# Kernel tuning notes

Hardware: AMD Instinct MI355X
Metric: run time of the kernel (lower is better)

## Reference

```python
import jax, jax.numpy as jnp
import numpy as np

N_QUBITS = 4
N_LAYERS = 2
BATCH = 262144


def _apply_ry(psi, theta, wire):
    # psi: (B, 2,2,2,2) real statevector; theta: scalar or (B,)
    c = jnp.reshape(jnp.cos(theta * 0.5), (-1, 1, 1, 1))
    s = jnp.reshape(jnp.sin(theta * 0.5), (-1, 1, 1, 1))
    psi = jnp.moveaxis(psi, wire + 1, 1)
    a, b = psi[:, 0], psi[:, 1]
    psi = jnp.stack([c * a - s * b, s * a + c * b], axis=1)
    return jnp.moveaxis(psi, 1, wire + 1)


def _apply_cnot(psi, ctrl, tgt):
    # flip target amplitude where control bit is 1
    psi = jnp.moveaxis(psi, (ctrl + 1, tgt + 1), (1, 2))
    psi = psi.at[:, 1].set(psi[:, 1, ::-1])
    return jnp.moveaxis(psi, (1, 2), (ctrl + 1, tgt + 1))


def _circuit(encoded, q_params):
    # Batched 4-qubit statevector sim (RY/CNOT are real matrices -> real psi).
    B = encoded.shape[0]
    psi = jnp.zeros((B, 2 ** N_QUBITS), encoded.dtype).at[:, 0].set(1.0)
    psi = psi.reshape((B,) + (2,) * N_QUBITS)  # wire 0 = most significant axis
    for w in range(N_QUBITS):
        psi = _apply_ry(psi, encoded[:, w], w)
    for layer in range(N_LAYERS):
        for i in range(N_QUBITS - 1):
            psi = _apply_cnot(psi, i, i + 1)
        psi = _apply_cnot(psi, N_QUBITS - 1, 0)  # ring closure (n_qubits > 2)
        for i in range(N_QUBITS):
            psi = _apply_ry(psi, q_params[layer * N_QUBITS + i], i)
    p = psi * psi  # probabilities
    zs = []
    for w in range(N_QUBITS):
        pw = jnp.moveaxis(p, w + 1, 1).reshape(B, 2, -1)
        zs.append(pw[:, 0].sum(-1) - pw[:, 1].sum(-1))  # <Z_w>
    return jnp.stack(zs, axis=-1)  # (B, 4)


def setup_inputs() -> dict:
    key = jax.random.key(0)
    ks = jax.random.split(key, 10)
    f32 = jnp.float32
    state = jax.random.normal(ks[0], (BATCH, 64), dtype=f32)
    # state_encoder: Linear(64,32) -> ReLU -> Linear(32,4) -> Tanh
    W1 = jax.random.normal(ks[1], (32, 64), dtype=f32) / np.sqrt(64.0)
    b1 = jnp.zeros((32,), f32)
    W2 = jax.random.normal(ks[2], (N_QUBITS, 32), dtype=f32) / np.sqrt(32.0)
    b2 = jnp.zeros((N_QUBITS,), f32)
    q_params = jax.random.normal(ks[3], (N_LAYERS * N_QUBITS,), dtype=f32) * 0.1
    # q_value_head: Linear(4,32) -> ReLU -> Linear(32,16) -> Tanh
    H1 = jax.random.normal(ks[4], (32, N_QUBITS), dtype=f32) / np.sqrt(float(N_QUBITS))
    c1 = jnp.zeros((32,), f32)
    H2 = jax.random.normal(ks[5], (16, 32), dtype=f32) / np.sqrt(32.0)
    c2 = jnp.zeros((16,), f32)
    return {"state": state, "W1": W1, "b1": b1, "W2": W2, "b2": b2,
            "q_params": q_params, "H1": H1, "c1": c1, "H2": H2, "c2": c2}


def reference(state, W1, b1, W2, b2, q_params, H1, c1, H2, c2):
    B = state.shape[0]
    x = state.reshape(B, -1)
    h = jax.nn.relu(x @ W1.T + b1)
    encoded = jnp.tanh(h @ W2.T + b2)            # (B, 4) rotation angles
    qf = _circuit(encoded, q_params)             # (B, 4) PauliZ expectations
    h2 = jax.nn.relu(qf @ H1.T + c1)
    q_values = jnp.tanh(h2 @ H2.T + c2)          # (B, 16)
    return q_values.reshape(B, 4, 4)
```

## Files before the change

kernel.cpp:

```cpp
#include <hip/hip_runtime.h>

#define TPB 256
#define BATCH 262144
#define S 34
#define EST 10
#define H2ST 36

typedef __fp16   fp16x2  __attribute__((ext_vector_type(2)));
typedef _Float16 half8_t __attribute__((ext_vector_type(8)));
typedef float    f32x4   __attribute__((ext_vector_type(4)));

#define WAVE_LDS_FENCE() asm volatile("s_waitcnt lgkmcnt(0)" ::: "memory")

__device__ __forceinline__ float fast_tanh(float x) {
    float ax = fabsf(x);
    float e  = __expf(-2.0f * ax);
    float t  = (1.0f - e) * __builtin_amdgcn_rcpf(1.0f + e);
    return copysignf(t, x);
}

template <int MASK>
__device__ __forceinline__ void ry_gate(float* psi, float c, float s) {
#pragma unroll
    for (int i = 0; i < 16; i++) {
        if (!(i & MASK)) {
            float a = psi[i], b = psi[i | MASK];
            psi[i]        = c * a - s * b;
            psi[i | MASK] = s * a + c * b;
        }
    }
}

template <int CM, int TM>
__device__ __forceinline__ void cnot_gate(float* psi) {
#pragma unroll
    for (int i = 0; i < 16; i++) {
        if ((i & CM) && !(i & TM)) {
            float t = psi[i];
            psi[i] = psi[i | TM];
            psi[i | TM] = t;
        }
    }
}

__device__ __forceinline__ half8_t cvt8(float4 a, float4 b) {
    fp16x2 p0 = __builtin_amdgcn_cvt_pkrtz(a.x, a.y);
    fp16x2 p1 = __builtin_amdgcn_cvt_pkrtz(a.z, a.w);
    fp16x2 p2 = __builtin_amdgcn_cvt_pkrtz(b.x, b.y);
    fp16x2 p3 = __builtin_amdgcn_cvt_pkrtz(b.z, b.w);
    half8_t r;
    r[0] = (_Float16)p0[0]; r[1] = (_Float16)p0[1];
    r[2] = (_Float16)p1[0]; r[3] = (_Float16)p1[1];
    r[4] = (_Float16)p2[0]; r[5] = (_Float16)p2[1];
    r[6] = (_Float16)p3[0]; r[7] = (_Float16)p3[1];
    return r;
}

__device__ __forceinline__ half8_t cvt8_rne(float4 a, float4 b) {
    half8_t r;
    r[0] = (_Float16)a.x; r[1] = (_Float16)a.y; r[2] = (_Float16)a.z; r[3] = (_Float16)a.w;
    r[4] = (_Float16)b.x; r[5] = (_Float16)b.y; r[6] = (_Float16)b.z; r[7] = (_Float16)b.w;
    return r;
}

__global__ __launch_bounds__(TPB, 4) void qnet_kernel(
    const float* __restrict__ state,
    const float* __restrict__ W1, const float* __restrict__ b1,
    const float* __restrict__ W2, const float* __restrict__ b2,
    const float* __restrict__ qp,
    const float* __restrict__ H1, const float* __restrict__ c1,
    const float* __restrict__ H2, const float* __restrict__ c2,
    float* __restrict__ out)
{
    __shared__ float sh[4 * 64 * S];

    const int tid  = threadIdx.x;
    const int lane = tid & 63;
    const int wv   = tid >> 6;
    const int l15  = lane & 15;
    const int lq   = lane >> 4;
    const int rowBase = blockIdx.x * TPB + wv * 64;
    float* hb = sh + wv * 64 * S;

    float4 xa[4][2], xb[4][2];
#pragma unroll
    for (int mt = 0; mt < 4; mt++) {
        const float* p0 = state + (size_t)(rowBase + 16 * mt + l15) * 64 + lq * 8;
#pragma unroll
        for (int kt = 0; kt < 2; kt++) {
            xa[mt][kt] = *(const float4*)(p0 + 32 * kt);
            xb[mt][kt] = *(const float4*)(p0 + 32 * kt + 4);
        }
    }

    half8_t bW1[2][2];
#pragma unroll
    for (int u = 0; u < 2; u++)
#pragma unroll
        for (int kt = 0; kt < 2; kt++) {
            const float* p = W1 + (16 * u + l15) * 64 + 32 * kt + lq * 8;
            bW1[u][kt] = cvt8(*(const float4*)p, *(const float4*)(p + 4));
        }
    const float bias0 = b1[l15];
    const float bias1 = b1[16 + l15];

    f32x4 acc[4][2];
#pragma unroll
    for (int mt = 0; mt < 4; mt++)
#pragma unroll
        for (int u = 0; u < 2; u++)
#pragma unroll
            for (int r = 0; r < 4; r++) acc[mt][u][r] = 0.0f;

#pragma unroll
    for (int kt = 0; kt < 2; kt++) {
#pragma unroll
        for (int mt = 0; mt < 4; mt++) {
            half8_t a = cvt8(xa[mt][kt], xb[mt][kt]);
            acc[mt][0] = __builtin_amdgcn_mfma_f32_16x16x32_f16(a, bW1[0][kt], acc[mt][0], 0, 0, 0);
            acc[mt][1] = __builtin_amdgcn_mfma_f32_16x16x32_f16(a, bW1[1][kt], acc[mt][1], 0, 0, 0);
        }
    }

#pragma unroll
    for (int mt = 0; mt < 4; mt++)
#pragma unroll
        for (int r = 0; r < 4; r++) {
            int row = 16 * mt + 4 * lq + r;
            hb[row * S + l15]      = fmaxf(acc[mt][0][r] + bias0, 0.0f);
            hb[row * S + 16 + l15] = fmaxf(acc[mt][1][r] + bias1, 0.0f);
        }
    WAVE_LDS_FENCE();

    half8_t bW2;
    {
        const float* p = W2 + (l15 & 3) * 32 + lq * 8;
        bW2 = cvt8_rne(*(const float4*)p, *(const float4*)(p + 4));
    }
    f32x4 eacc[4];
#pragma unroll
    for (int mt = 0; mt < 4; mt++) {
#pragma unroll
        for (int r = 0; r < 4; r++) eacc[mt][r] = 0.0f;
        const float2* q = reinterpret_cast<const float2*>(hb + (16 * mt + l15) * S + lq * 8);
        float2 a0 = q[0], a1 = q[1], a2 = q[2], a3 = q[3];
        half8_t a = cvt8_rne(make_float4(a0.x, a0.y, a1.x, a1.y),
                             make_float4(a2.x, a2.y, a3.x, a3.y));
        eacc[mt] = __builtin_amdgcn_mfma_f32_16x16x32_f16(a, bW2, eacc[mt], 0, 0, 0);
    }
    WAVE_LDS_FENCE();

    if (l15 < 4) {
#pragma unroll
        for (int mt = 0; mt < 4; mt++)
#pragma unroll
            for (int r = 0; r < 4; r++)
                hb[(16 * mt + 4 * lq + r) * EST + l15] = eacc[mt][r];
    }
    WAVE_LDS_FENCE();

    float e[4];
    {
        const float2* ep = reinterpret_cast<const float2*>(hb + lane * EST);
        float2 v0 = ep[0], v1 = ep[1];
        e[0] = fast_tanh(v0.x + b2[0]);
        e[1] = fast_tanh(v0.y + b2[1]);
        e[2] = fast_tanh(v1.x + b2[2]);
        e[3] = fast_tanh(v1.y + b2[3]);
    }

    float qf[4];
    {
        float sn[4], cs[4];
#pragma unroll
        for (int w = 0; w < 4; w++) __sincosf(0.5f * e[w], &sn[w], &cs[w]);
        float t01[4] = { cs[0]*cs[1], cs[0]*sn[1], sn[0]*cs[1], sn[0]*sn[1] };
        float t23[4] = { cs[2]*cs[3], cs[2]*sn[3], sn[2]*cs[3], sn[2]*sn[3] };
        float psi[16];
#pragma unroll
        for (int i = 0; i < 16; i++) psi[i] = t01[i >> 2] * t23[i & 3];

#pragma unroll
        for (int layer = 0; layer < 2; layer++) {
            cnot_gate<8, 4>(psi);
            cnot_gate<4, 2>(psi);
            cnot_gate<2, 1>(psi);
            cnot_gate<1, 8>(psi);
#pragma unroll
            for (int i = 0; i < 4; i++) {
                float s2, c2v;
                __sincosf(0.5f * qp[layer * 4 + i], &s2, &c2v);
                if (i == 0) ry_gate<8>(psi, c2v, s2);
                if (i == 1) ry_gate<4>(psi, c2v, s2);
                if (i == 2) ry_gate<2>(psi, c2v, s2);
                if (i == 3) ry_gate<1>(psi, c2v, s2);
            }
        }

        float p_[16];
#pragma unroll
        for (int i = 0; i < 16; i++) p_[i] = psi[i] * psi[i];
        float d0 = p_[0] - p_[8],  d1 = p_[1] - p_[9];
        float d2 = p_[2] - p_[10], d3 = p_[3] - p_[11];
        float d4 = p_[4] - p_[12], d5 = p_[5] - p_[13];
        float d6 = p_[6] - p_[14], d7 = p_[7] - p_[15];
        qf[0] = ((d0 + d1) + (d2 + d3)) + ((d4 + d5) + (d6 + d7));
        float s0 = p_[0] + p_[8],  s1 = p_[1] + p_[9];
        float s2 = p_[2] + p_[10], s3 = p_[3] + p_[11];
        float s4 = p_[4] + p_[12], s5 = p_[5] + p_[13];
        float s6 = p_[6] + p_[14], s7 = p_[7] + p_[15];
        qf[1] = ((s0 - s4) + (s1 - s5)) + ((s2 - s6) + (s3 - s7));
        float u0 = s0 + s4, u1 = s1 + s5, u2 = s2 + s6, u3 = s3 + s7;
        qf[2] = (u0 - u2) + (u1 - u3);
        qf[3] = (u0 + u2) - (u1 + u3);
    }

    float h2v[32];
#pragma unroll
    for (int j = 0; j < 32; j++) {
        float a = c1[j];
        a = fmaf(qf[0], H1[j * 4 + 0], a);
        a = fmaf(qf[1], H1[j * 4 + 1], a);
        a = fmaf(qf[2], H1[j * 4 + 2], a);
        a = fmaf(qf[3], H1[j * 4 + 3], a);
        h2v[j] = fmaxf(a, 0.0f);
    }

    {
        uint2* wp = reinterpret_cast<uint2*>(
            reinterpret_cast<__fp16*>(hb) + (size_t)lane * H2ST);
#pragma unroll
        for (int j = 0; j < 8; j++) {
            fp16x2 q0 = __builtin_amdgcn_cvt_pkrtz(h2v[4 * j],     h2v[4 * j + 1]);
            fp16x2 q1 = __builtin_amdgcn_cvt_pkrtz(h2v[4 * j + 2], h2v[4 * j + 3]);
            wp[j] = make_uint2(__builtin_bit_cast(unsigned int, q0),
                               __builtin_bit_cast(unsigned int, q1));
        }
    }
    WAVE_LDS_FENCE();

    half8_t bH2;
    {
        const float* p = H2 + l15 * 32 + lq * 8;
        bH2 = cvt8(*(const float4*)p, *(const float4*)(p + 4));
    }

    f32x4 acc2[4];
#pragma unroll
    for (int mt = 0; mt < 4; mt++) {
#pragma unroll
        for (int r = 0; r < 4; r++) acc2[mt][r] = 0.0f;
        const __fp16* rp = reinterpret_cast<const __fp16*>(hb)
                         + (16 * mt + l15) * H2ST + lq * 8;
        uint2 wlo = *reinterpret_cast<const uint2*>(rp);
        uint2 whi = *reinterpret_cast<const uint2*>(rp + 4);
        half8_t a = __builtin_bit_cast(half8_t, make_uint4(wlo.x, wlo.y, whi.x, whi.y));
        acc2[mt] = __builtin_amdgcn_mfma_f32_16x16x32_f16(a, bH2, acc2[mt], 0, 0, 0);
    }

    const float cc = c2[l15];
#pragma unroll
    for (int mt = 0; mt < 4; mt++)
#pragma unroll
        for (int r = 0; r < 4; r++) {
            int row = rowBase + 16 * mt + 4 * lq + r;
            out[(size_t)row * 16 + l15] = fast_tanh(acc2[mt][r] + cc);
        }
}

extern "C" void kernel_launch(void* const* d_in, const int* in_sizes, int n_in,
                              void* d_out, int out_size, void* d_ws, size_t ws_size,
                              hipStream_t stream) {
    const float* state = (const float*)d_in[0];
    const float* W1    = (const float*)d_in[1];
    const float* b1    = (const float*)d_in[2];
    const float* W2    = (const float*)d_in[3];
    const float* b2    = (const float*)d_in[4];
    const float* qp    = (const float*)d_in[5];
    const float* H1    = (const float*)d_in[6];
    const float* c1    = (const float*)d_in[7];
    const float* H2    = (const float*)d_in[8];
    const float* c2    = (const float*)d_in[9];
    float* out = (float*)d_out;

    const int blocks = BATCH / TPB;
    qnet_kernel<<<blocks, TPB, 0, stream>>>(state, W1, b1, W2, b2, qp,
                                            H1, c1, H2, c2, out);
}
```

Baseline: 122.1 us.

## Store hidden activations as fp16 in LDS, hoist weight loads, and use nontemporal state loads

The ReLU hidden layer is now written to LDS as fp16 with a 40-element stride, so the second matmul reads one 16-byte half8 vector instead of converting float pairs. The encoded values go to a separate LDS region, which removes one wave fence. All weight and bias loads, plus the sin/cos of the circuit parameters (moved to scalar registers), are hoisted to the start so their latency overlaps with the nontemporal loads of the streamed state rows, which are issued in two halves. The second-layer input rounding changes from round-to-nearest to round-toward-zero, and more values are live in registers early on.

Result: slower. 125.3 us (+2.6%).

```diff
diff --git a/kernel.cpp b/kernel.cpp
--- a/kernel.cpp
+++ b/kernel.cpp
@@ -2,9 +2,10 @@
 
 #define TPB 256
 #define BATCH 262144
-#define S 34
+#define HST 40
 #define EST 10
-#define H2ST 36
+#define HREG 1280
+#define SLICE 1920
 
 typedef __fp16   fp16x2  __attribute__((ext_vector_type(2)));
 typedef _Float16 half8_t __attribute__((ext_vector_type(8)));
@@ -19,6 +20,10 @@
     return copysignf(t, x);
 }
 
+__device__ __forceinline__ float to_sgpr(float v) {
+    return __builtin_bit_cast(float, __builtin_amdgcn_readfirstlane(__builtin_bit_cast(int, v)));
+}
+
 template <int MASK>
 __device__ __forceinline__ void ry_gate(float* psi, float c, float s) {
 #pragma unroll
@@ -43,23 +48,16 @@
     }
 }
 
-__device__ __forceinline__ half8_t cvt8(float4 a, float4 b) {
-    fp16x2 p0 = __builtin_amdgcn_cvt_pkrtz(a.x, a.y);
-    fp16x2 p1 = __builtin_amdgcn_cvt_pkrtz(a.z, a.w);
-    fp16x2 p2 = __builtin_amdgcn_cvt_pkrtz(b.x, b.y);
-    fp16x2 p3 = __builtin_amdgcn_cvt_pkrtz(b.z, b.w);
+__device__ __forceinline__ half8_t cvt8(f32x4 a, f32x4 b) {
+    fp16x2 p0 = __builtin_amdgcn_cvt_pkrtz(a[0], a[1]);
+    fp16x2 p1 = __builtin_amdgcn_cvt_pkrtz(a[2], a[3]);
+    fp16x2 p2 = __builtin_amdgcn_cvt_pkrtz(b[0], b[1]);
+    fp16x2 p3 = __builtin_amdgcn_cvt_pkrtz(b[2], b[3]);
     half8_t r;
     r[0] = (_Float16)p0[0]; r[1] = (_Float16)p0[1];
     r[2] = (_Float16)p1[0]; r[3] = (_Float16)p1[1];
     r[4] = (_Float16)p2[0]; r[5] = (_Float16)p2[1];
     r[6] = (_Float16)p3[0]; r[7] = (_Float16)p3[1];
-    return r;
-}
-
-__device__ __forceinline__ half8_t cvt8_rne(float4 a, float4 b) {
-    half8_t r;
-    r[0] = (_Float16)a.x; r[1] = (_Float16)a.y; r[2] = (_Float16)a.z; r[3] = (_Float16)a.w;
-    r[4] = (_Float16)b.x; r[5] = (_Float16)b.y; r[6] = (_Float16)b.z; r[7] = (_Float16)b.w;
     return r;
 }
 
@@ -72,7 +70,7 @@
     const float* __restrict__ H2, const float* __restrict__ c2,
     float* __restrict__ out)
 {
-    __shared__ float sh[4 * 64 * S];
+    __shared__ float sh[4 * SLICE];
 
     const int tid  = threadIdx.x;
     const int lane = tid & 63;
@@ -80,29 +78,67 @@
     const int l15  = lane & 15;
     const int lq   = lane >> 4;
     const int rowBase = blockIdx.x * TPB + wv * 64;
-    float* hb = sh + wv * 64 * S;
-
-    float4 xa[4][2], xb[4][2];
+    float*  hb   = sh + wv * SLICE;
+    __fp16* hb16 = reinterpret_cast<__fp16*>(hb);
+    float*  eb   = hb + HREG;
+
+    f32x4 xa0[4], xb0[4];
 #pragma unroll
     for (int mt = 0; mt < 4; mt++) {
         const float* p0 = state + (size_t)(rowBase + 16 * mt + l15) * 64 + lq * 8;
-#pragma unroll
-        for (int kt = 0; kt < 2; kt++) {
-            xa[mt][kt] = *(const float4*)(p0 + 32 * kt);
-            xb[mt][kt] = *(const float4*)(p0 + 32 * kt + 4);
-        }
-    }
-
-    half8_t bW1[2][2];
+        xa0[mt] = __builtin_nontemporal_load(reinterpret_cast<const f32x4*>(p0));
+        xb0[mt] = __builtin_nontemporal_load(reinterpret_cast<const f32x4*>(p0 + 4));
+    }
+
+    f32x4 w1a[2][2], w1b[2][2];
 #pragma unroll
     for (int u = 0; u < 2; u++)
 #pragma unroll
         for (int kt = 0; kt < 2; kt++) {
             const float* p = W1 + (16 * u + l15) * 64 + 32 * kt + lq * 8;
-            bW1[u][kt] = cvt8(*(const float4*)p, *(const float4*)(p + 4));
-        }
+            w1a[u][kt] = *reinterpret_cast<const f32x4*>(p);
+            w1b[u][kt] = *reinterpret_cast<const f32x4*>(p + 4);
+        }
+    f32x4 w2a, w2b, h2wa, h2wb;
+    {
+        const float* p = W2 + (l15 & 3) * 32 + lq * 8;
+        w2a = *reinterpret_cast<const f32x4*>(p);
+        w2b = *reinterpret_cast<const f32x4*>(p + 4);
+        const float* q = H2 + l15 * 32 + lq * 8;
+        h2wa = *reinterpret_cast<const f32x4*>(q);
+        h2wb = *reinterpret_cast<const f32x4*>(q + 4);
+    }
     const float bias0 = b1[l15];
     const float bias1 = b1[16 + l15];
+    const float cc    = c2[l15];
+
+    float qpc[8], qps[8];
+#pragma unroll
+    for (int g = 0; g < 8; g++) {
+        float sg, cg;
+        __sincosf(0.5f * qp[g], &sg, &cg);
+        qps[g] = to_sgpr(sg);
+        qpc[g] = to_sgpr(cg);
+    }
+
+    half8_t aft[4];
+#pragma unroll
+    for (int mt = 0; mt < 4; mt++) aft[mt] = cvt8(xa0[mt], xb0[mt]);
+
+    f32x4 xa1[4], xb1[4];
+#pragma unroll
+    for (int mt = 0; mt < 4; mt++) {
+        const float* p0 = state + (size_t)(rowBase + 16 * mt + l15) * 64 + 32 + lq * 8;
+        xa1[mt] = __builtin_nontemporal_load(reinterpret_cast<const f32x4*>(p0));
+        xb1[mt] = __builtin_nontemporal_load(reinterpret_cast<const f32x4*>(p0 + 4));
+    }
+
+    half8_t bW1[2][2];
+#pragma unroll
+    for (int u = 0; u < 2; u++)
+#pragma unroll
+        for (int kt = 0; kt < 2; kt++)
+            bW1[u][kt] = cvt8(w1a[u][kt], w1b[u][kt]);
 
     f32x4 acc[4][2];
 #pragma unroll
@@ -113,13 +149,15 @@
             for (int r = 0; r < 4; r++) acc[mt][u][r] = 0.0f;
 
 #pragma unroll
-    for (int kt = 0; kt < 2; kt++) {
-#pragma unroll
-        for (int mt = 0; mt < 4; mt++) {
-            half8_t a = cvt8(xa[mt][kt], xb[mt][kt]);
-            acc[mt][0] = __builtin_amdgcn_mfma_f32_16x16x32_f16(a, bW1[0][kt], acc[mt][0], 0, 0, 0);
-            acc[mt][1] = __builtin_amdgcn_mfma_f32_16x16x32_f16(a, bW1[1][kt], acc[mt][1], 0, 0, 0);
-        }
+    for (int mt = 0; mt < 4; mt++) {
+        acc[mt][0] = __builtin_amdgcn_mfma_f32_16x16x32_f16(aft[mt], bW1[0][0], acc[mt][0], 0, 0, 0);
+        acc[mt][1] = __builtin_amdgcn_mfma_f32_16x16x32_f16(aft[mt], bW1[1][0], acc[mt][1], 0, 0, 0);
+    }
+#pragma unroll
+    for (int mt = 0; mt < 4; mt++) {
+        half8_t a = cvt8(xa1[mt], xb1[mt]);
+        acc[mt][0] = __builtin_amdgcn_mfma_f32_16x16x32_f16(a, bW1[0][1], acc[mt][0], 0, 0, 0);
+        acc[mt][1] = __builtin_amdgcn_mfma_f32_16x16x32_f16(a, bW1[1][1], acc[mt][1], 0, 0, 0);
     }
 
 #pragma unroll
@@ -127,41 +165,33 @@
 #pragma unroll
         for (int r = 0; r < 4; r++) {
             int row = 16 * mt + 4 * lq + r;
-            hb[row * S + l15]      = fmaxf(acc[mt][0][r] + bias0, 0.0f);
-            hb[row * S + 16 + l15] = fmaxf(acc[mt][1][r] + bias1, 0.0f);
+            hb16[row * HST + l15]      = (__fp16)fmaxf(acc[mt][0][r] + bias0, 0.0f);
+            hb16[row * HST + 16 + l15] = (__fp16)fmaxf(acc[mt][1][r] + bias1, 0.0f);
         }
     WAVE_LDS_FENCE();
 
-    half8_t bW2;
-    {
-        const float* p = W2 + (l15 & 3) * 32 + lq * 8;
-        bW2 = cvt8_rne(*(const float4*)p, *(const float4*)(p + 4));
-    }
+    half8_t bW2 = cvt8(w2a, w2b);
     f32x4 eacc[4];
 #pragma unroll
     for (int mt = 0; mt < 4; mt++) {
 #pragma unroll
         for (int r = 0; r < 4; r++) eacc[mt][r] = 0.0f;
-        const float2* q = reinterpret_cast<const float2*>(hb + (16 * mt + l15) * S + lq * 8);
-        float2 a0 = q[0], a1 = q[1], a2 = q[2], a3 = q[3];
-        half8_t a = cvt8_rne(make_float4(a0.x, a0.y, a1.x, a1.y),
-                             make_float4(a2.x, a2.y, a3.x, a3.y));
+        half8_t a = *reinterpret_cast<const half8_t*>(hb16 + (16 * mt + l15) * HST + lq * 8);
         eacc[mt] = __builtin_amdgcn_mfma_f32_16x16x32_f16(a, bW2, eacc[mt], 0, 0, 0);
     }
-    WAVE_LDS_FENCE();
 
     if (l15 < 4) {
 #pragma unroll
         for (int mt = 0; mt < 4; mt++)
 #pragma unroll
             for (int r = 0; r < 4; r++)
-                hb[(16 * mt + 4 * lq + r) * EST + l15] = eacc[mt][r];
+                eb[(16 * mt + 4 * lq + r) * EST + l15] = eacc[mt][r];
     }
     WAVE_LDS_FENCE();
 
     float e[4];
     {
-        const float2* ep = reinterpret_cast<const float2*>(hb + lane * EST);
+        const float2* ep = reinterpret_cast<const float2*>(eb + lane * EST);
         float2 v0 = ep[0], v1 = ep[1];
         e[0] = fast_tanh(v0.x + b2[0]);
         e[1] = fast_tanh(v0.y + b2[1]);
@@ -186,15 +216,10 @@
             cnot_gate<4, 2>(psi);
             cnot_gate<2, 1>(psi);
             cnot_gate<1, 8>(psi);
-#pragma unroll
-            for (int i = 0; i < 4; i++) {
-                float s2, c2v;
-                __sincosf(0.5f * qp[layer * 4 + i], &s2, &c2v);
-                if (i == 0) ry_gate<8>(psi, c2v, s2);
-                if (i == 1) ry_gate<4>(psi, c2v, s2);
-                if (i == 2) ry_gate<2>(psi, c2v, s2);
-                if (i == 3) ry_gate<1>(psi, c2v, s2);
-            }
+            ry_gate<8>(psi, qpc[layer * 4 + 0], qps[layer * 4 + 0]);
+            ry_gate<4>(psi, qpc[layer * 4 + 1], qps[layer * 4 + 1]);
+            ry_gate<2>(psi, qpc[layer * 4 + 2], qps[layer * 4 + 2]);
+            ry_gate<1>(psi, qpc[layer * 4 + 3], qps[layer * 4 + 3]);
         }
 
         float p_[16];
@@ -227,8 +252,7 @@
     }
 
     {
-        uint2* wp = reinterpret_cast<uint2*>(
-            reinterpret_cast<__fp16*>(hb) + (size_t)lane * H2ST);
+        uint2* wp = reinterpret_cast<uint2*>(hb16 + (size_t)lane * HST);
 #pragma unroll
         for (int j = 0; j < 8; j++) {
             fp16x2 q0 = __builtin_amdgcn_cvt_pkrtz(h2v[4 * j],     h2v[4 * j + 1]);
@@ -239,26 +263,16 @@
     }
     WAVE_LDS_FENCE();
 
-    half8_t bH2;
-    {
-        const float* p = H2 + l15 * 32 + lq * 8;
-        bH2 = cvt8(*(const float4*)p, *(const float4*)(p + 4));
-    }
-
+    half8_t bH2 = cvt8(h2wa, h2wb);
     f32x4 acc2[4];
 #pragma unroll
     for (int mt = 0; mt < 4; mt++) {
 #pragma unroll
         for (int r = 0; r < 4; r++) acc2[mt][r] = 0.0f;
-        const __fp16* rp = reinterpret_cast<const __fp16*>(hb)
-                         + (16 * mt + l15) * H2ST + lq * 8;
-        uint2 wlo = *reinterpret_cast<const uint2*>(rp);
-        uint2 whi = *reinterpret_cast<const uint2*>(rp + 4);
-        half8_t a = __builtin_bit_cast(half8_t, make_uint4(wlo.x, wlo.y, whi.x, whi.y));
+        half8_t a = *reinterpret_cast<const half8_t*>(hb16 + (16 * mt + l15) * HST + lq * 8);
         acc2[mt] = __builtin_amdgcn_mfma_f32_16x16x32_f16(a, bH2, acc2[mt], 0, 0, 0);
     }
 
-    const float cc = c2[l15];
 #pragma unroll
     for (int mt = 0; mt < 4; mt++)
 #pragma unroll
```
